# Kernel optimization log

Hardware: AMD Instinct MI355X
Metric: run time of the kernel (lower is better)

## Reference

```python
import jax, jax.numpy as jnp
import numpy as np
from jax import lax

EPS = 1e-5
DN = ('NCHW', 'OIHW', 'NCHW')


def setup_inputs() -> dict:
    key = jax.random.key(0)
    ks = jax.random.split(key, 16)
    B = 8192
    # uniform(0,1): every pixel nonzero => all voxels active => sparse conv == dense conv
    x = jax.random.uniform(ks[0], (B, 1, 28, 28), dtype=jnp.float32)

    def conv_params(kw, kb, c_in, c_out, k):
        scale = 1.0 / np.sqrt(c_in * k * k)
        w = jax.random.normal(kw, (c_out, c_in, k, k), dtype=jnp.float32) * scale
        b = jax.random.normal(kb, (c_out,), dtype=jnp.float32) * scale
        return w, b

    w0, b0 = conv_params(ks[1], ks[2], 1, 32, 3)
    w1, b1 = conv_params(ks[3], ks[4], 32, 64, 2)
    w2, b2 = conv_params(ks[5], ks[6], 64, 128, 2)
    # BatchNorm affine params (init: gamma=1, beta=0)
    g0, be0 = jnp.ones((32,), jnp.float32), jnp.zeros((32,), jnp.float32)
    g1, be1 = jnp.ones((64,), jnp.float32), jnp.zeros((64,), jnp.float32)
    g2, be2 = jnp.ones((128,), jnp.float32), jnp.zeros((128,), jnp.float32)
    w_fc = jax.random.normal(ks[7], (10, 128), dtype=jnp.float32) * (1.0 / np.sqrt(128))
    b_fc = jax.random.normal(ks[8], (10,), dtype=jnp.float32) * (1.0 / np.sqrt(128))
    return dict(x=x, w0=w0, b0=b0, g0=g0, be0=be0,
                w1=w1, b1=b1, g1=g1, be1=be1,
                w2=w2, b2=b2, g2=g2, be2=be2,
                w_fc=w_fc, b_fc=b_fc)


def _conv_bn_relu(x, w, b, g, be, stride, padding):
    # sparse conv on fully-active grid == dense conv
    y = lax.conv_general_dilated(x, w, (stride, stride), padding,
                                 dimension_numbers=DN)
    y = y + b[None, :, None, None]
    # BatchNorm1d over (N_active, C) == stats over batch+spatial (biased var)
    mean = jnp.mean(y, axis=(0, 2, 3))
    var = jnp.var(y, axis=(0, 2, 3))
    y = (y - mean[None, :, None, None]) * lax.rsqrt(var + EPS)[None, :, None, None]
    y = y * g[None, :, None, None] + be[None, :, None, None]
    return jax.nn.relu(y)


def reference(x, w0, b0, g0, be0, w1, b1, g1, be1, w2, b2, g2, be2, w_fc, b_fc):
    h = _conv_bn_relu(x, w0, b0, g0, be0, 1, 'SAME')    # (B,32,28,28)
    h = _conv_bn_relu(h, w1, b1, g1, be1, 2, 'VALID')   # (B,64,14,14)
    h = _conv_bn_relu(h, w2, b2, g2, be2, 2, 'VALID')   # (B,128,7,7)
    pooled = jnp.mean(h, axis=(2, 3))                    # AdaptiveAvgPool2d(1)+Flatten
    return pooled @ w_fc.T + b_fc                        # (B, n_classes)
```

## Files before the change

### kernel.cpp

```cpp
#include <hip/hip_runtime.h>
#include <hip/hip_bf16.h>

typedef __bf16 bf16x8 __attribute__((ext_vector_type(8)));
typedef float  f32x4  __attribute__((ext_vector_type(4)));
typedef float  f32x2  __attribute__((ext_vector_type(2)));

#define BSZ 8192

__device__ __constant__ int d_base2[9] = {0, 5, 9, 13, 16, 19, 21, 23, 24};

__global__ __launch_bounds__(256) void k_stats0(const float* __restrict__ x,
                                                float* __restrict__ part0,
                                                const float* __restrict__ w1,
                                                const float* __restrict__ w2,
                                                __bf16* __restrict__ w1b,
                                                __bf16* __restrict__ w2b) {
    __shared__ float sred[4 * 59];
    const int tid = threadIdx.x;
    {
        int t = blockIdx.x * 256 + tid;
        if (t < 8192) {
            int oc = t >> 7, k = t & 127, c = k & 31, d = k >> 5;
            w1b[t] = (__bf16)w1[oc * 128 + c * 4 + d];
        }
        if (t < 32768) {
            int oc = t >> 8, k = t & 255, c = k & 63, d = k >> 6;
            w2b[t] = (__bf16)w2[oc * 256 + c * 4 + d];
        }
    }
    const int base2[9] = {0, 5, 9, 13, 16, 19, 21, 23, 24};
    const int rsz[9]   = {5, 4, 4, 3, 3, 2, 2, 1, 1};
    f32x2 a2[25];
    float ax[9];
#pragma unroll
    for (int i = 0; i < 25; i++) a2[i] = (f32x2){0.f, 0.f};
#pragma unroll
    for (int i = 0; i < 9; i++) ax[i] = 0.f;
    const int total = BSZ * 784;
    for (int p = blockIdx.x * 256 + tid; p < total; p += gridDim.x * 256) {
        int b = p / 784, pix = p - b * 784;
        int y = pix / 28, xx = pix - y * 28;
        const float* xb = x + (long)b * 784;
        float nv[9];
#pragma unroll
        for (int dy = 0; dy < 3; dy++) {
            int yy = y + dy - 1;
#pragma unroll
            for (int dx = 0; dx < 3; dx++) {
                int x2 = xx + dx - 1;
                nv[dy * 3 + dx] = (yy >= 0 && yy < 28 && x2 >= 0 && x2 < 28) ? xb[yy * 28 + x2] : 0.f;
            }
        }
#pragma unroll
        for (int t = 0; t < 9; t++) {
            float vt = nv[t];
            ax[t] += vt;
            f32x2 vv = {vt, vt};
#pragma unroll
            for (int pp2 = 0; pp2 < 5; pp2++) {
                if (pp2 < rsz[t]) {
                    int u = t + 2 * pp2;
                    f32x2 nn = {nv[u], (u + 1 < 9) ? nv[u + 1] : 0.f};
                    a2[base2[t] + pp2] = __builtin_elementwise_fma(vv, nn, a2[base2[t] + pp2]);
                }
            }
        }
    }
    float outv[59];
#pragma unroll
    for (int i = 0; i < 50; i++) outv[i] = a2[i >> 1][i & 1];
#pragma unroll
    for (int i = 0; i < 9; i++) outv[50 + i] = ax[i];
#pragma unroll
    for (int i = 0; i < 59; i++) {
        float v = outv[i];
        v += __shfl_xor(v, 1);  v += __shfl_xor(v, 2);  v += __shfl_xor(v, 4);
        v += __shfl_xor(v, 8);  v += __shfl_xor(v, 16); v += __shfl_xor(v, 32);
        outv[i] = v;
    }
    const int l = tid & 63, w = tid >> 6;
    if (l == 0) {
#pragma unroll
        for (int i = 0; i < 59; i++) sred[w * 59 + i] = outv[i];
    }
    __syncthreads();
    if (tid < 59)
        part0[blockIdx.x * 64 + tid] = sred[tid] + sred[59 + tid] + sred[118 + tid] + sred[177 + tid];
}

__global__ void k_fin0(const float* __restrict__ part0, const float* __restrict__ w0,
                       const float* __restrict__ g0, const float* __restrict__ be0,
                       float* __restrict__ abc0) {
    __shared__ float red[4 * 59];
    int t = threadIdx.x, c = t & 63, g = t >> 6;
    if (c < 59) {
        float acc = 0.f;
        for (int i = g; i < 1024; i += 4) acc += part0[i * 64 + c];
        red[g * 59 + c] = acc;
    }
    __syncthreads();
    if (t < 59) red[t] = red[t] + red[59 + t] + red[118 + t] + red[177 + t];
    __syncthreads();
    if (t < 32) {
        const int base2[9] = {0, 5, 9, 13, 16, 19, 21, 23, 24};
        float wv[9];
#pragma unroll
        for (int tap = 0; tap < 9; tap++) wv[tap] = w0[t * 9 + tap];
        float sum = 0.f, sq = 0.f;
#pragma unroll
        for (int ta = 0; ta < 9; ta++) {
            sum = fmaf(wv[ta], red[50 + ta], sum);
#pragma unroll
            for (int u = ta; u < 9; u++) {
                float coef = (u == ta) ? 1.f : 2.f;
                float Mv = red[2 * base2[ta] + (u - ta)];
                sq = fmaf(coef * wv[ta] * wv[u], Mv, sq);
            }
        }
        float cnt = (float)BSZ * 784.f;
        float mean = sum / cnt;
        float var = sq / cnt - mean * mean;
        float A = g0[t] * rsqrtf(var + 1e-5f);
#pragma unroll
        for (int tap = 0; tap < 9; tap++)
            abc0[(t >> 3) * 72 + tap * 8 + (t & 7)] = A * wv[tap];
        abc0[288 + t] = be0[t] - mean * A;
    }
}

__global__ __launch_bounds__(256) void k_conv01(const float* __restrict__ x,
                                                const float* __restrict__ abc0,
                                                const __bf16* __restrict__ w1b,
                                                __bf16* __restrict__ h1,
                                                float* __restrict__ part1) {
    __shared__ float xs[30 * 30];
    __shared__ __attribute__((aligned(16))) __bf16 sAt[2][16 * 136];
    const int tid = threadIdx.x;
    if (tid < 116) {
        int idx;
        if (tid < 30)      idx = tid;
        else if (tid < 60) idx = 29 * 30 + (tid - 30);
        else if (tid < 88) idx = (tid - 60 + 1) * 30;
        else               idx = (tid - 88 + 1) * 30 + 29;
        xs[idx] = 0.f;
    }
    const int pgu = __builtin_amdgcn_readfirstlane(tid >> 6);
    const f32x2* wfp = (const f32x2*)(abc0 + pgu * 72);
    f32x2 wf2[36];
#pragma unroll
    for (int i = 0; i < 36; i++) wf2[i] = wfp[i];
    const f32x2* c2p = (const f32x2*)(abc0 + 288 + pgu * 8);
    f32x2 c2[4];
#pragma unroll
    for (int j = 0; j < 4; j++) c2[j] = c2p[j];

    const int pi = tid & 15, pd = (tid >> 4) & 3;
    const int w = tid >> 6, l = tid & 63, q = l >> 4, n = l & 15;
    const int oc = w * 16 + n;
    bf16x8 fbv[4];
#pragma unroll
    for (int kc = 0; kc < 4; kc++)
        fbv[kc] = *(const bf16x8*)&w1b[oc * 128 + kc * 32 + q * 8];
    const f32x2 zero2 = {0.f, 0.f};

    for (int img = 0; img < 4; img++) {
        const int b = blockIdx.x * 4 + img;
        const f32x4* xb4 = (const f32x4*)(x + (long)b * 784);
        if (tid < 196) {
            int yy = tid / 7, xx4 = (tid - yy * 7) * 4;
            f32x4 v4 = xb4[tid];
            float* dst = &xs[(yy + 1) * 30 + xx4 + 1];
            dst[0] = v4[0]; dst[1] = v4[1]; dst[2] = v4[2]; dst[3] = v4[3];
        }
        __syncthreads();
        f32x2 st_s = zero2, st_q = zero2;
        __bf16* hb = h1 + (long)b * 12544 + (q * 4) * 64 + oc;
        for (int mt = 0; mt < 13; mt++) {
            __bf16* dst = &sAt[mt & 1][pi * 136 + pd * 32 + pgu * 8];
            int m = mt * 16 + pi;
            bf16x8 pk;
            if (m < 196) {
                int my = m / 14, mx = m - my * 14;
                int y0 = my * 2 + (pd >> 1), x0 = mx * 2 + (pd & 1);
                float nv[9];
#pragma unroll
                for (int dy = 0; dy < 3; dy++)
#pragma unroll
                    for (int dx = 0; dx < 3; dx++)
                        nv[dy * 3 + dx] = xs[(y0 + dy) * 30 + x0 + dx];
                f32x2 a2[4];
#pragma unroll
                for (int j = 0; j < 4; j++) a2[j] = c2[j];
#pragma unroll
                for (int t = 0; t < 9; t++) {
                    f32x2 vv = {nv[t], nv[t]};
#pragma unroll
                    for (int j = 0; j < 4; j++)
                        a2[j] = __builtin_elementwise_fma(vv, wf2[t * 4 + j], a2[j]);
                }
#pragma unroll
                for (int j = 0; j < 4; j++) {
                    f32x2 mv = __builtin_elementwise_max(a2[j], zero2);
                    pk[2 * j]     = (__bf16)mv[0];
                    pk[2 * j + 1] = (__bf16)mv[1];
                }
            } else {
#pragma unroll
                for (int j = 0; j < 8; j++) pk[j] = (__bf16)0.0f;
            }
            *(bf16x8*)dst = pk;
            __syncthreads();
            const __bf16* sa = &sAt[mt & 1][n * 136 + q * 8];
            f32x4 acc = {0.f, 0.f, 0.f, 0.f};
#pragma unroll
            for (int kc = 0; kc < 4; kc++) {
                bf16x8 fav = *(const bf16x8*)&sa[kc * 32];
                acc = __builtin_amdgcn_mfma_f32_16x16x32_bf16(fav, fbv[kc], acc, 0, 0, 0);
            }
            bool valid = (mt < 12) | (q == 0);
            __bf16* hp = hb + mt * 16 * 64;
            float fv[4];
#pragma unroll
            for (int r = 0; r < 4; r++) {
                __bf16 hv = (__bf16)acc[r];
                if (valid) hp[r * 64] = hv;
                fv[r] = (float)hv;
            }
            f32x2 f01 = {fv[0], fv[1]}, f23 = {fv[2], fv[3]};
            st_s = st_s + f01; st_s = st_s + f23;
            st_q = __builtin_elementwise_fma(f01, f01, st_q);
            st_q = __builtin_elementwise_fma(f23, f23, st_q);
        }
        float ssum = st_s[0] + st_s[1], ssq = st_q[0] + st_q[1];
        ssum += __shfl_xor(ssum, 16); ssum += __shfl_xor(ssum, 32);
        ssq  += __shfl_xor(ssq, 16);  ssq  += __shfl_xor(ssq, 32);
        if (l < 16) {
            part1[(long)oc * BSZ + b] = ssum;
            part1[(long)(64 + oc) * BSZ + b] = ssq;
        }
    }
}

__global__ __launch_bounds__(256) void k_redfin(const float* __restrict__ part,
                                                const float* __restrict__ g,
                                                const float* __restrict__ be,
                                                float* __restrict__ abc,
                                                int C, float cnt) {
    __shared__ float s1[256], s2[256];
    const int c = blockIdx.x, tid = threadIdx.x;
    float a = 0.f, bq = 0.f;
    const float* p1 = part + (long)c * BSZ;
    const float* p2 = part + (long)(C + c) * BSZ;
    for (int i = tid; i < BSZ; i += 256) { a += p1[i]; bq += p2[i]; }
    s1[tid] = a; s2[tid] = bq;
    __syncthreads();
    for (int s = 128; s > 0; s >>= 1) {
        if (tid < s) { s1[tid] += s1[tid + s]; s2[tid] += s2[tid + s]; }
        __syncthreads();
    }
    if (tid == 0) {
        float mean = s1[0] / cnt;
        float var = s2[0] / cnt - mean * mean;
        float A = g[c] * rsqrtf(var + 1e-5f);
        abc[c] = A;
        abc[C + c] = be[c] - mean * A;
    }
}

__global__ __launch_bounds__(256) void k_conv2s(__bf16* __restrict__ h1,
                                                const __bf16* __restrict__ w2b,
                                                const float* __restrict__ abc1,
                                                float* __restrict__ part2) {
    __shared__ __attribute__((aligned(16))) __bf16 sAt[2][16 * 264];
    __shared__ __attribute__((aligned(16))) __bf16 zt[2][16 * 136];
    __shared__ float sbn1[128];
    const int tid = threadIdx.x;
    if (tid < 128) sbn1[tid] = abc1[tid];
    const int w = tid >> 6, l = tid & 63, q = l >> 4, n = l & 15;
    bf16x8 fbv[2][8];
#pragma unroll
    for (int ntl = 0; ntl < 2; ntl++) {
        int oc = (2 * w + ntl) * 16 + n;
#pragma unroll
        for (int kc = 0; kc < 8; kc++)
            fbv[ntl][kc] = *(const bf16x8*)&w2b[oc * 256 + kc * 32 + q * 8];
    }
    __syncthreads();
    const int cpb = (tid & 7) * 8;
    f32x2 A1p[4], C1p[4];
#pragma unroll
    for (int p = 0; p < 4; p++) {
        A1p[p] = (f32x2){sbn1[cpb + 2 * p], sbn1[cpb + 2 * p + 1]};
        C1p[p] = (f32x2){sbn1[64 + cpb + 2 * p], sbn1[64 + cpb + 2 * p + 1]};
    }
    const f32x2 zero2 = {0.f, 0.f};
    const int srow = tid >> 4, so = (tid & 15) * 8;

    for (int img = 0; img < 4; img++) {
        const int b = blockIdx.x * 4 + img;
        __bf16* src = h1 + (long)b * 12544;
        f32x2 st_s[2] = {zero2, zero2}, st_q[2] = {zero2, zero2};
        for (int mt = 0; mt < 4; mt++) {
            if (mt >= 2) {
                int m = (mt - 2) * 16 + srow;
                if (m < 49) {
                    bf16x8 zv = *(const bf16x8*)&zt[mt & 1][srow * 136 + so];
                    *(bf16x8*)&src[m * 128 + so] = zv;
                }
            }
#pragma unroll
            for (int it = 0; it < 2; it++) {
                int idx = it * 256 + tid;
                int rl = idx >> 5, o = (idx & 31) * 8;
                int r = mt * 16 + rl;
                bf16x8 wv;
                if (r < 49) {
                    int d = o >> 6;
                    int c = o & 63;
                    int py = r / 7, px = r - py * 7;
                    int msrc = (2 * py + (d >> 1)) * 14 + 2 * px + (d & 1);
                    bf16x8 v = *(const bf16x8*)&src[msrc * 64 + c];
#pragma unroll
                    for (int p = 0; p < 4; p++) {
                        f32x2 vf = {(float)v[2 * p], (float)v[2 * p + 1]};
                        f32x2 rr = __builtin_elementwise_fma(vf, A1p[p], C1p[p]);
                        rr = __builtin_elementwise_max(rr, zero2);
                        wv[2 * p]     = (__bf16)rr[0];
                        wv[2 * p + 1] = (__bf16)rr[1];
                    }
                } else {
#pragma unroll
                    for (int j = 0; j < 8; j++) wv[j] = (__bf16)0.0f;
                }
                *(bf16x8*)&sAt[mt & 1][rl * 264 + o] = wv;
            }
            __syncthreads();
            bf16x8 fav[8];
#pragma unroll
            for (int kc = 0; kc < 8; kc++)
                fav[kc] = *(const bf16x8*)&sAt[mt & 1][n * 264 + kc * 32 + q * 8];
#pragma unroll
            for (int ntl = 0; ntl < 2; ntl++) {
                f32x4 acc = {0.f, 0.f, 0.f, 0.f};
#pragma unroll
                for (int kc = 0; kc < 8; kc++)
                    acc = __builtin_amdgcn_mfma_f32_16x16x32_bf16(fav[kc], fbv[ntl][kc], acc, 0, 0, 0);
                float fv[4];
#pragma unroll
                for (int rr = 0; rr < 4; rr++) {
                    __bf16 hv = (__bf16)acc[rr];
                    zt[mt & 1][(q * 4 + rr) * 136 + (2 * w + ntl) * 16 + n] = hv;
                    fv[rr] = (float)hv;
                }
                f32x2 f01 = {fv[0], fv[1]}, f23 = {fv[2], fv[3]};
                st_s[ntl] = st_s[ntl] + f01; st_s[ntl] = st_s[ntl] + f23;
                st_q[ntl] = __builtin_elementwise_fma(f01, f01, st_q[ntl]);
                st_q[ntl] = __builtin_elementwise_fma(f23, f23, st_q[ntl]);
            }
        }
        __syncthreads();
        {
            int m2 = 32 + srow;
            if (m2 < 49) {
                bf16x8 zv = *(const bf16x8*)&zt[0][srow * 136 + so];
                *(bf16x8*)&src[m2 * 128 + so] = zv;
            }
            int m3 = 48 + srow;
            if (m3 < 49) {
                bf16x8 zv = *(const bf16x8*)&zt[1][srow * 136 + so];
                *(bf16x8*)&src[m3 * 128 + so] = zv;
            }
        }
#pragma unroll
        for (int ntl = 0; ntl < 2; ntl++) {
            float ssum = st_s[ntl][0] + st_s[ntl][1];
            float ssq  = st_q[ntl][0] + st_q[ntl][1];
            ssum += __shfl_xor(ssum, 16); ssum += __shfl_xor(ssum, 32);
            ssq  += __shfl_xor(ssq, 16);  ssq  += __shfl_xor(ssq, 32);
            if (l < 16) {
                int oc = (2 * w + ntl) * 16 + l;
                part2[(long)oc * BSZ + b] = ssum;
                part2[(long)(128 + oc) * BSZ + b] = ssq;
            }
        }
    }
}

__global__ __launch_bounds__(256) void k_final(const __bf16* __restrict__ z2,
                                               const float* __restrict__ abc2,
                                               const float* __restrict__ wfc,
                                               const float* __restrict__ bfc,
                                               float* __restrict__ out) {
    __shared__ float sbn2[256];
    __shared__ float pp[16 * 128];
    __shared__ float pooled[128];
    __shared__ float fcred[80];
    const int tid = threadIdx.x;
    sbn2[tid] = abc2[tid];
    __syncthreads();
    const int g = tid & 15, c0 = g * 8, rg = tid >> 4;
    f32x2 A2p[4], C2p[4];
#pragma unroll
    for (int p = 0; p < 4; p++) {
        A2p[p] = (f32x2){sbn2[c0 + 2 * p], sbn2[c0 + 2 * p + 1]};
        C2p[p] = (f32x2){sbn2[128 + c0 + 2 * p], sbn2[128 + c0 + 2 * p + 1]};
    }
    const f32x2 zero2 = {0.f, 0.f};
    for (int img = 0; img < 4; img++) {
        const int b = blockIdx.x * 4 + img;
        const __bf16* src = z2 + (long)b * 12544;
        f32x2 acc2[4];
#pragma unroll
        for (int p = 0; p < 4; p++) acc2[p] = zero2;
        for (int rr = rg; rr < 49; rr += 16) {
            bf16x8 v = *(const bf16x8*)&src[rr * 128 + c0];
#pragma unroll
            for (int p = 0; p < 4; p++) {
                f32x2 vf = {(float)v[2 * p], (float)v[2 * p + 1]};
                f32x2 t0 = __builtin_elementwise_fma(vf, A2p[p], C2p[p]);
                t0 = __builtin_elementwise_max(t0, zero2);
                acc2[p] = acc2[p] + t0;
            }
        }
        f32x4 lo = {acc2[0][0], acc2[0][1], acc2[1][0], acc2[1][1]};
        f32x4 hi = {acc2[2][0], acc2[2][1], acc2[3][0], acc2[3][1]};
        *(f32x4*)&pp[rg * 128 + c0]     = lo;
        *(f32x4*)&pp[rg * 128 + c0 + 4] = hi;
        __syncthreads();
        if (tid < 128) {
            float s = 0.f;
#pragma unroll
            for (int r = 0; r < 16; r++) s += pp[r * 128 + tid];
            pooled[tid] = s * (1.f / 49.f);
        }
        __syncthreads();
        if (tid < 80) {
            int o = tid >> 3, s = tid & 7;
            float a = 0.f;
#pragma unroll
            for (int j = 0; j < 16; j++) a = fmaf(pooled[s * 16 + j], wfc[o * 128 + s * 16 + j], a);
            fcred[tid] = a;
        }
        __syncthreads();
        if (tid < 10) {
            float a = bfc[tid];
#pragma unroll
            for (int s = 0; s < 8; s++) a += fcred[tid * 8 + s];
            out[(long)b * 10 + tid] = a;
        }
    }
}

extern "C" void kernel_launch(void* const* d_in, const int* in_sizes, int n_in,
                              void* d_out, int out_size, void* d_ws, size_t ws_size,
                              hipStream_t stream) {
    const float* x   = (const float*)d_in[0];
    const float* w0  = (const float*)d_in[1];
    const float* g0  = (const float*)d_in[3];
    const float* be0 = (const float*)d_in[4];
    const float* w1  = (const float*)d_in[5];
    const float* g1  = (const float*)d_in[7];
    const float* be1 = (const float*)d_in[8];
    const float* w2  = (const float*)d_in[9];
    const float* g2  = (const float*)d_in[11];
    const float* be2 = (const float*)d_in[12];
    const float* wfc = (const float*)d_in[13];
    const float* bfc = (const float*)d_in[14];
    float* out = (float*)d_out;

    float* ws    = (float*)d_ws;
    float* part0 = ws;
    float* abc0  = part0 + 1024 * 64;
    float* part1 = abc0 + 320;
    float* abc1  = part1 + 128 * BSZ;
    float* part2 = abc1 + 128;
    float* abc2  = part2 + 256 * BSZ;
    __bf16* w1b  = (__bf16*)(abc2 + 256);
    __bf16* w2b  = w1b + 8192;
    __bf16* h1   = w2b + 32768;

    k_stats0<<<dim3(1024), dim3(256), 0, stream>>>(x, part0, w1, w2, w1b, w2b);
    k_fin0<<<dim3(1), dim3(256), 0, stream>>>(part0, w0, g0, be0, abc0);
    k_conv01<<<dim3(BSZ / 4), dim3(256), 0, stream>>>(x, abc0, w1b, h1, part1);
    k_redfin<<<dim3(64), dim3(256), 0, stream>>>(part1, g1, be1, abc1, 64, (float)(BSZ * 196));
    k_conv2s<<<dim3(BSZ / 4), dim3(256), 0, stream>>>(h1, w2b, abc1, part2);
    k_redfin<<<dim3(128), dim3(256), 0, stream>>>(part2, g2, be2, abc2, 128, (float)(BSZ * 49));
    k_final<<<dim3(BSZ / 4), dim3(256), 0, stream>>>(h1, abc2, wfc, bfc, out);
}
```

Baseline: 410.3 us.

## Fuse all stages into one cooperative persistent kernel with grid syncs

Replaces the seven separate kernel launches with a single cooperative kernel of 512 persistent blocks. Each block handles 16 images, and stages are separated by grid.sync. Per-image partial statistics are now accumulated per block, which shrinks the partial buffers and the final reductions. This removes launch gaps and per-launch overhead. In exchange, grid-wide barriers are added and occupancy is capped by the 4-blocks-per-CU launch bound, which may reduce latency hiding during the heavy conv stages.

```diff
diff --git a/kernel.cpp b/kernel.cpp
--- a/kernel.cpp
+++ b/kernel.cpp
@@ -1,374 +1,390 @@
 #include <hip/hip_runtime.h>
 #include <hip/hip_bf16.h>
+#include <hip/hip_cooperative_groups.h>
+
+namespace cg = cooperative_groups;
 
 typedef __bf16 bf16x8 __attribute__((ext_vector_type(8)));
 typedef float  f32x4  __attribute__((ext_vector_type(4)));
 typedef float  f32x2  __attribute__((ext_vector_type(2)));
 
 #define BSZ 8192
-
-__device__ __constant__ int d_base2[9] = {0, 5, 9, 13, 16, 19, 21, 23, 24};
-
-__global__ __launch_bounds__(256) void k_stats0(const float* __restrict__ x,
-                                                float* __restrict__ part0,
-                                                const float* __restrict__ w1,
-                                                const float* __restrict__ w2,
-                                                __bf16* __restrict__ w1b,
-                                                __bf16* __restrict__ w2b) {
-    __shared__ float sred[4 * 59];
-    const int tid = threadIdx.x;
+#define NBLK 512
+#define IPB  16
+
+__global__ __launch_bounds__(256, 4) void k_mega(const float* __restrict__ x,
+                                                 const float* __restrict__ w0,
+                                                 const float* __restrict__ g0,
+                                                 const float* __restrict__ be0,
+                                                 const float* __restrict__ w1,
+                                                 const float* __restrict__ g1,
+                                                 const float* __restrict__ be1,
+                                                 const float* __restrict__ w2,
+                                                 const float* __restrict__ g2,
+                                                 const float* __restrict__ be2,
+                                                 const float* __restrict__ wfc,
+                                                 const float* __restrict__ bfc,
+                                                 float* __restrict__ out,
+                                                 float* __restrict__ wsf) {
+    __shared__ __attribute__((aligned(16))) unsigned char smem[26112];
+    cg::grid_group grid = cg::this_grid();
+    const int tid = threadIdx.x, blk = blockIdx.x;
+
+    float* part0 = wsf;
+    float* abc0  = part0 + NBLK * 64;
+    float* part1 = abc0 + 320;
+    float* abc1  = part1 + 128 * NBLK;
+    float* part2 = abc1 + 128;
+    float* abc2  = part2 + 256 * NBLK;
+    __bf16* w1b  = (__bf16*)(abc2 + 256);
+    __bf16* w2b  = w1b + 8192;
+    __bf16* h1   = w2b + 32768;
+
     {
-        int t = blockIdx.x * 256 + tid;
-        if (t < 8192) {
-            int oc = t >> 7, k = t & 127, c = k & 31, d = k >> 5;
-            w1b[t] = (__bf16)w1[oc * 128 + c * 4 + d];
-        }
-        if (t < 32768) {
-            int oc = t >> 8, k = t & 255, c = k & 63, d = k >> 6;
-            w2b[t] = (__bf16)w2[oc * 256 + c * 4 + d];
-        }
-    }
-    const int base2[9] = {0, 5, 9, 13, 16, 19, 21, 23, 24};
-    const int rsz[9]   = {5, 4, 4, 3, 3, 2, 2, 1, 1};
-    f32x2 a2[25];
-    float ax[9];
-#pragma unroll
-    for (int i = 0; i < 25; i++) a2[i] = (f32x2){0.f, 0.f};
-#pragma unroll
-    for (int i = 0; i < 9; i++) ax[i] = 0.f;
-    const int total = BSZ * 784;
-    for (int p = blockIdx.x * 256 + tid; p < total; p += gridDim.x * 256) {
-        int b = p / 784, pix = p - b * 784;
-        int y = pix / 28, xx = pix - y * 28;
-        const float* xb = x + (long)b * 784;
-        float nv[9];
-#pragma unroll
-        for (int dy = 0; dy < 3; dy++) {
-            int yy = y + dy - 1;
-#pragma unroll
-            for (int dx = 0; dx < 3; dx++) {
-                int x2 = xx + dx - 1;
-                nv[dy * 3 + dx] = (yy >= 0 && yy < 28 && x2 >= 0 && x2 < 28) ? xb[yy * 28 + x2] : 0.f;
-            }
-        }
-#pragma unroll
-        for (int t = 0; t < 9; t++) {
-            float vt = nv[t];
-            ax[t] += vt;
-            f32x2 vv = {vt, vt};
-#pragma unroll
-            for (int pp2 = 0; pp2 < 5; pp2++) {
-                if (pp2 < rsz[t]) {
-                    int u = t + 2 * pp2;
-                    f32x2 nn = {nv[u], (u + 1 < 9) ? nv[u + 1] : 0.f};
-                    a2[base2[t] + pp2] = __builtin_elementwise_fma(vv, nn, a2[base2[t] + pp2]);
-                }
-            }
-        }
-    }
-    float outv[59];
-#pragma unroll
-    for (int i = 0; i < 50; i++) outv[i] = a2[i >> 1][i & 1];
-#pragma unroll
-    for (int i = 0; i < 9; i++) outv[50 + i] = ax[i];
-#pragma unroll
-    for (int i = 0; i < 59; i++) {
-        float v = outv[i];
-        v += __shfl_xor(v, 1);  v += __shfl_xor(v, 2);  v += __shfl_xor(v, 4);
-        v += __shfl_xor(v, 8);  v += __shfl_xor(v, 16); v += __shfl_xor(v, 32);
-        outv[i] = v;
-    }
-    const int l = tid & 63, w = tid >> 6;
-    if (l == 0) {
-#pragma unroll
-        for (int i = 0; i < 59; i++) sred[w * 59 + i] = outv[i];
-    }
-    __syncthreads();
-    if (tid < 59)
-        part0[blockIdx.x * 64 + tid] = sred[tid] + sred[59 + tid] + sred[118 + tid] + sred[177 + tid];
-}
-
-__global__ void k_fin0(const float* __restrict__ part0, const float* __restrict__ w0,
-                       const float* __restrict__ g0, const float* __restrict__ be0,
-                       float* __restrict__ abc0) {
-    __shared__ float red[4 * 59];
-    int t = threadIdx.x, c = t & 63, g = t >> 6;
-    if (c < 59) {
-        float acc = 0.f;
-        for (int i = g; i < 1024; i += 4) acc += part0[i * 64 + c];
-        red[g * 59 + c] = acc;
-    }
-    __syncthreads();
-    if (t < 59) red[t] = red[t] + red[59 + t] + red[118 + t] + red[177 + t];
-    __syncthreads();
-    if (t < 32) {
+        float* sred = (float*)smem;
+        for (int t = blk * 256 + tid; t < 32768; t += NBLK * 256) {
+            if (t < 8192) {
+                int oc = t >> 7, k = t & 127, c = k & 31, d = k >> 5;
+                w1b[t] = (__bf16)w1[oc * 128 + c * 4 + d];
+            }
+            {
+                int oc = t >> 8, k = t & 255, c = k & 63, d = k >> 6;
+                w2b[t] = (__bf16)w2[oc * 256 + c * 4 + d];
+            }
+        }
         const int base2[9] = {0, 5, 9, 13, 16, 19, 21, 23, 24};
-        float wv[9];
-#pragma unroll
-        for (int tap = 0; tap < 9; tap++) wv[tap] = w0[t * 9 + tap];
-        float sum = 0.f, sq = 0.f;
-#pragma unroll
-        for (int ta = 0; ta < 9; ta++) {
-            sum = fmaf(wv[ta], red[50 + ta], sum);
-#pragma unroll
-            for (int u = ta; u < 9; u++) {
-                float coef = (u == ta) ? 1.f : 2.f;
-                float Mv = red[2 * base2[ta] + (u - ta)];
-                sq = fmaf(coef * wv[ta] * wv[u], Mv, sq);
-            }
-        }
-        float cnt = (float)BSZ * 784.f;
-        float mean = sum / cnt;
-        float var = sq / cnt - mean * mean;
-        float A = g0[t] * rsqrtf(var + 1e-5f);
-#pragma unroll
-        for (int tap = 0; tap < 9; tap++)
-            abc0[(t >> 3) * 72 + tap * 8 + (t & 7)] = A * wv[tap];
-        abc0[288 + t] = be0[t] - mean * A;
-    }
-}
-
-__global__ __launch_bounds__(256) void k_conv01(const float* __restrict__ x,
-                                                const float* __restrict__ abc0,
-                                                const __bf16* __restrict__ w1b,
-                                                __bf16* __restrict__ h1,
-                                                float* __restrict__ part1) {
-    __shared__ float xs[30 * 30];
-    __shared__ __attribute__((aligned(16))) __bf16 sAt[2][16 * 136];
-    const int tid = threadIdx.x;
-    if (tid < 116) {
-        int idx;
-        if (tid < 30)      idx = tid;
-        else if (tid < 60) idx = 29 * 30 + (tid - 30);
-        else if (tid < 88) idx = (tid - 60 + 1) * 30;
-        else               idx = (tid - 88 + 1) * 30 + 29;
-        xs[idx] = 0.f;
-    }
-    const int pgu = __builtin_amdgcn_readfirstlane(tid >> 6);
-    const f32x2* wfp = (const f32x2*)(abc0 + pgu * 72);
-    f32x2 wf2[36];
-#pragma unroll
-    for (int i = 0; i < 36; i++) wf2[i] = wfp[i];
-    const f32x2* c2p = (const f32x2*)(abc0 + 288 + pgu * 8);
-    f32x2 c2[4];
-#pragma unroll
-    for (int j = 0; j < 4; j++) c2[j] = c2p[j];
-
-    const int pi = tid & 15, pd = (tid >> 4) & 3;
-    const int w = tid >> 6, l = tid & 63, q = l >> 4, n = l & 15;
-    const int oc = w * 16 + n;
-    bf16x8 fbv[4];
-#pragma unroll
-    for (int kc = 0; kc < 4; kc++)
-        fbv[kc] = *(const bf16x8*)&w1b[oc * 128 + kc * 32 + q * 8];
-    const f32x2 zero2 = {0.f, 0.f};
-
-    for (int img = 0; img < 4; img++) {
-        const int b = blockIdx.x * 4 + img;
-        const f32x4* xb4 = (const f32x4*)(x + (long)b * 784);
-        if (tid < 196) {
-            int yy = tid / 7, xx4 = (tid - yy * 7) * 4;
-            f32x4 v4 = xb4[tid];
-            float* dst = &xs[(yy + 1) * 30 + xx4 + 1];
-            dst[0] = v4[0]; dst[1] = v4[1]; dst[2] = v4[2]; dst[3] = v4[3];
-        }
-        __syncthreads();
+        const int rsz[9]   = {5, 4, 4, 3, 3, 2, 2, 1, 1};
+        f32x2 a2[25];
+        float ax[9];
+#pragma unroll
+        for (int i = 0; i < 25; i++) a2[i] = (f32x2){0.f, 0.f};
+#pragma unroll
+        for (int i = 0; i < 9; i++) ax[i] = 0.f;
+        const int total = BSZ * 784;
+        for (int p = blk * 256 + tid; p < total; p += NBLK * 256) {
+            int b = p / 784, pix = p - b * 784;
+            int y = pix / 28, xx = pix - y * 28;
+            const float* xb = x + (long)b * 784;
+            float nv[9];
+#pragma unroll
+            for (int dy = 0; dy < 3; dy++) {
+                int yy = y + dy - 1;
+#pragma unroll
+                for (int dx = 0; dx < 3; dx++) {
+                    int x2 = xx + dx - 1;
+                    nv[dy * 3 + dx] = (yy >= 0 && yy < 28 && x2 >= 0 && x2 < 28) ? xb[yy * 28 + x2] : 0.f;
+                }
+            }
+#pragma unroll
+            for (int t2 = 0; t2 < 9; t2++) {
+                float vt = nv[t2];
+                ax[t2] += vt;
+                f32x2 vv = {vt, vt};
+#pragma unroll
+                for (int pp2 = 0; pp2 < 5; pp2++) {
+                    if (pp2 < rsz[t2]) {
+                        int u = t2 + 2 * pp2;
+                        f32x2 nn = {nv[u], (u + 1 < 9) ? nv[u + 1] : 0.f};
+                        a2[base2[t2] + pp2] = __builtin_elementwise_fma(vv, nn, a2[base2[t2] + pp2]);
+                    }
+                }
+            }
+        }
+        float outv[59];
+#pragma unroll
+        for (int i = 0; i < 50; i++) outv[i] = a2[i >> 1][i & 1];
+#pragma unroll
+        for (int i = 0; i < 9; i++) outv[50 + i] = ax[i];
+#pragma unroll
+        for (int i = 0; i < 59; i++) {
+            float v = outv[i];
+            v += __shfl_xor(v, 1);  v += __shfl_xor(v, 2);  v += __shfl_xor(v, 4);
+            v += __shfl_xor(v, 8);  v += __shfl_xor(v, 16); v += __shfl_xor(v, 32);
+            outv[i] = v;
+        }
+        const int l = tid & 63, w = tid >> 6;
+        if (l == 0) {
+#pragma unroll
+            for (int i = 0; i < 59; i++) sred[w * 59 + i] = outv[i];
+        }
+        __syncthreads();
+        if (tid < 59)
+            part0[blk * 64 + tid] = sred[tid] + sred[59 + tid] + sred[118 + tid] + sred[177 + tid];
+    }
+    grid.sync();
+
+    if (blk == 0) {
+        float* red = (float*)smem;
+        int t = tid, c = t & 63, g = t >> 6;
+        if (c < 59) {
+            float acc = 0.f;
+            for (int i = g; i < NBLK; i += 4) acc += part0[i * 64 + c];
+            red[g * 59 + c] = acc;
+        }
+        __syncthreads();
+        if (t < 59) red[t] = red[t] + red[59 + t] + red[118 + t] + red[177 + t];
+        __syncthreads();
+        if (t < 32) {
+            const int base2[9] = {0, 5, 9, 13, 16, 19, 21, 23, 24};
+            float wv[9];
+#pragma unroll
+            for (int tap = 0; tap < 9; tap++) wv[tap] = w0[t * 9 + tap];
+            float sum = 0.f, sq = 0.f;
+#pragma unroll
+            for (int ta = 0; ta < 9; ta++) {
+                sum = fmaf(wv[ta], red[50 + ta], sum);
+#pragma unroll
+                for (int u = ta; u < 9; u++) {
+                    float coef = (u == ta) ? 1.f : 2.f;
+                    float Mv = red[2 * base2[ta] + (u - ta)];
+                    sq = fmaf(coef * wv[ta] * wv[u], Mv, sq);
+                }
+            }
+            float cnt = (float)BSZ * 784.f;
+            float mean = sum / cnt;
+            float var = sq / cnt - mean * mean;
+            float A = g0[t] * rsqrtf(var + 1e-5f);
+#pragma unroll
+            for (int tap = 0; tap < 9; tap++)
+                abc0[(t >> 3) * 72 + tap * 8 + (t & 7)] = A * wv[tap];
+            abc0[288 + t] = be0[t] - mean * A;
+        }
+    }
+    grid.sync();
+
+    {
+        float* xs = (float*)smem;
+        __bf16* sAt = (__bf16*)(smem + 3600);
+        if (tid < 116) {
+            int idx;
+            if (tid < 30)      idx = tid;
+            else if (tid < 60) idx = 29 * 30 + (tid - 30);
+            else if (tid < 88) idx = (tid - 60 + 1) * 30;
+            else               idx = (tid - 88 + 1) * 30 + 29;
+            xs[idx] = 0.f;
+        }
+        const int pgu = __builtin_amdgcn_readfirstlane(tid >> 6);
+        const f32x2* wfp = (const f32x2*)(abc0 + pgu * 72);
+        f32x2 wf2[36];
+#pragma unroll
+        for (int i = 0; i < 36; i++) wf2[i] = wfp[i];
+        const f32x2* c2p = (const f32x2*)(abc0 + 288 + pgu * 8);
+        f32x2 c2[4];
+#pragma unroll
+        for (int j = 0; j < 4; j++) c2[j] = c2p[j];
+        const int pi = tid & 15, pd = (tid >> 4) & 3;
+        const int w = tid >> 6, l = tid & 63, q = l >> 4, n = l & 15;
+        const int oc = w * 16 + n;
+        bf16x8 fbv[4];
+#pragma unroll
+        for (int kc = 0; kc < 4; kc++)
+            fbv[kc] = *(const bf16x8*)&w1b[oc * 128 + kc * 32 + q * 8];
+        const f32x2 zero2 = {0.f, 0.f};
         f32x2 st_s = zero2, st_q = zero2;
-        __bf16* hb = h1 + (long)b * 12544 + (q * 4) * 64 + oc;
-        for (int mt = 0; mt < 13; mt++) {
-            __bf16* dst = &sAt[mt & 1][pi * 136 + pd * 32 + pgu * 8];
-            int m = mt * 16 + pi;
-            bf16x8 pk;
-            if (m < 196) {
-                int my = m / 14, mx = m - my * 14;
-                int y0 = my * 2 + (pd >> 1), x0 = mx * 2 + (pd & 1);
-                float nv[9];
-#pragma unroll
-                for (int dy = 0; dy < 3; dy++)
-#pragma unroll
-                    for (int dx = 0; dx < 3; dx++)
-                        nv[dy * 3 + dx] = xs[(y0 + dy) * 30 + x0 + dx];
-                f32x2 a2[4];
-#pragma unroll
-                for (int j = 0; j < 4; j++) a2[j] = c2[j];
-#pragma unroll
-                for (int t = 0; t < 9; t++) {
-                    f32x2 vv = {nv[t], nv[t]};
-#pragma unroll
-                    for (int j = 0; j < 4; j++)
-                        a2[j] = __builtin_elementwise_fma(vv, wf2[t * 4 + j], a2[j]);
-                }
-#pragma unroll
-                for (int j = 0; j < 4; j++) {
-                    f32x2 mv = __builtin_elementwise_max(a2[j], zero2);
-                    pk[2 * j]     = (__bf16)mv[0];
-                    pk[2 * j + 1] = (__bf16)mv[1];
-                }
-            } else {
-#pragma unroll
-                for (int j = 0; j < 8; j++) pk[j] = (__bf16)0.0f;
-            }
-            *(bf16x8*)dst = pk;
-            __syncthreads();
-            const __bf16* sa = &sAt[mt & 1][n * 136 + q * 8];
-            f32x4 acc = {0.f, 0.f, 0.f, 0.f};
-#pragma unroll
-            for (int kc = 0; kc < 4; kc++) {
-                bf16x8 fav = *(const bf16x8*)&sa[kc * 32];
-                acc = __builtin_amdgcn_mfma_f32_16x16x32_bf16(fav, fbv[kc], acc, 0, 0, 0);
-            }
-            bool valid = (mt < 12) | (q == 0);
-            __bf16* hp = hb + mt * 16 * 64;
-            float fv[4];
-#pragma unroll
-            for (int r = 0; r < 4; r++) {
-                __bf16 hv = (__bf16)acc[r];
-                if (valid) hp[r * 64] = hv;
-                fv[r] = (float)hv;
-            }
-            f32x2 f01 = {fv[0], fv[1]}, f23 = {fv[2], fv[3]};
-            st_s = st_s + f01; st_s = st_s + f23;
-            st_q = __builtin_elementwise_fma(f01, f01, st_q);
-            st_q = __builtin_elementwise_fma(f23, f23, st_q);
+
+        for (int img = 0; img < IPB; img++) {
+            const int b = blk * IPB + img;
+            const f32x4* xb4 = (const f32x4*)(x + (long)b * 784);
+            if (tid < 196) {
+                int yy = tid / 7, xx4 = (tid - yy * 7) * 4;
+                f32x4 v4 = xb4[tid];
+                float* dst = &xs[(yy + 1) * 30 + xx4 + 1];
+                dst[0] = v4[0]; dst[1] = v4[1]; dst[2] = v4[2]; dst[3] = v4[3];
+            }
+            __syncthreads();
+            __bf16* hb = h1 + (long)b * 12544 + (q * 4) * 64 + oc;
+            for (int mt = 0; mt < 13; mt++) {
+                __bf16* dst = &sAt[(mt & 1) * 2176 + pi * 136 + pd * 32 + pgu * 8];
+                int m = mt * 16 + pi;
+                bf16x8 pk;
+                if (m < 196) {
+                    int my = m / 14, mx = m - my * 14;
+                    int y0 = my * 2 + (pd >> 1), x0 = mx * 2 + (pd & 1);
+                    float nv[9];
+#pragma unroll
+                    for (int dy = 0; dy < 3; dy++)
+#pragma unroll
+                        for (int dx = 0; dx < 3; dx++)
+                            nv[dy * 3 + dx] = xs[(y0 + dy) * 30 + x0 + dx];
+                    f32x2 a2[4];
+#pragma unroll
+                    for (int j = 0; j < 4; j++) a2[j] = c2[j];
+#pragma unroll
+                    for (int t = 0; t < 9; t++) {
+                        f32x2 vv = {nv[t], nv[t]};
+#pragma unroll
+                        for (int j = 0; j < 4; j++)
+                            a2[j] = __builtin_elementwise_fma(vv, wf2[t * 4 + j], a2[j]);
+                    }
+#pragma unroll
+                    for (int j = 0; j < 4; j++) {
+                        f32x2 mv = __builtin_elementwise_max(a2[j], zero2);
+                        pk[2 * j]     = (__bf16)mv[0];
+                        pk[2 * j + 1] = (__bf16)mv[1];
+                    }
+                } else {
+#pragma unroll
+                    for (int j = 0; j < 8; j++) pk[j] = (__bf16)0.0f;
+                }
+                *(bf16x8*)dst = pk;
+                __syncthreads();
+                const __bf16* sa = &sAt[(mt & 1) * 2176 + n * 136 + q * 8];
+                f32x4 acc = {0.f, 0.f, 0.f, 0.f};
+#pragma unroll
+                for (int kc = 0; kc < 4; kc++) {
+                    bf16x8 fav = *(const bf16x8*)&sa[kc * 32];
+                    acc = __builtin_amdgcn_mfma_f32_16x16x32_bf16(fav, fbv[kc], acc, 0, 0, 0);
+                }
+                bool valid = (mt < 12) | (q == 0);
+                __bf16* hp = hb + mt * 16 * 64;
+                float fv[4];
+#pragma unroll
+                for (int r = 0; r < 4; r++) {
+                    __bf16 hv = (__bf16)acc[r];
+                    if (valid) hp[r * 64] = hv;
+                    fv[r] = (float)hv;
+                }
+                f32x2 f01 = {fv[0], fv[1]}, f23 = {fv[2], fv[3]};
+                st_s = st_s + f01; st_s = st_s + f23;
+                st_q = __builtin_elementwise_fma(f01, f01, st_q);
+                st_q = __builtin_elementwise_fma(f23, f23, st_q);
+            }
+            __syncthreads();
         }
         float ssum = st_s[0] + st_s[1], ssq = st_q[0] + st_q[1];
         ssum += __shfl_xor(ssum, 16); ssum += __shfl_xor(ssum, 32);
         ssq  += __shfl_xor(ssq, 16);  ssq  += __shfl_xor(ssq, 32);
         if (l < 16) {
-            part1[(long)oc * BSZ + b] = ssum;
-            part1[(long)(64 + oc) * BSZ + b] = ssq;
-        }
-    }
-}
-
-__global__ __launch_bounds__(256) void k_redfin(const float* __restrict__ part,
-                                                const float* __restrict__ g,
-                                                const float* __restrict__ be,
-                                                float* __restrict__ abc,
-                                                int C, float cnt) {
-    __shared__ float s1[256], s2[256];
-    const int c = blockIdx.x, tid = threadIdx.x;
-    float a = 0.f, bq = 0.f;
-    const float* p1 = part + (long)c * BSZ;
-    const float* p2 = part + (long)(C + c) * BSZ;
-    for (int i = tid; i < BSZ; i += 256) { a += p1[i]; bq += p2[i]; }
-    s1[tid] = a; s2[tid] = bq;
-    __syncthreads();
-    for (int s = 128; s > 0; s >>= 1) {
-        if (tid < s) { s1[tid] += s1[tid + s]; s2[tid] += s2[tid + s]; }
-        __syncthreads();
-    }
-    if (tid == 0) {
-        float mean = s1[0] / cnt;
-        float var = s2[0] / cnt - mean * mean;
-        float A = g[c] * rsqrtf(var + 1e-5f);
-        abc[c] = A;
-        abc[C + c] = be[c] - mean * A;
-    }
-}
-
-__global__ __launch_bounds__(256) void k_conv2s(__bf16* __restrict__ h1,
-                                                const __bf16* __restrict__ w2b,
-                                                const float* __restrict__ abc1,
-                                                float* __restrict__ part2) {
-    __shared__ __attribute__((aligned(16))) __bf16 sAt[2][16 * 264];
-    __shared__ __attribute__((aligned(16))) __bf16 zt[2][16 * 136];
-    __shared__ float sbn1[128];
-    const int tid = threadIdx.x;
-    if (tid < 128) sbn1[tid] = abc1[tid];
-    const int w = tid >> 6, l = tid & 63, q = l >> 4, n = l & 15;
-    bf16x8 fbv[2][8];
-#pragma unroll
-    for (int ntl = 0; ntl < 2; ntl++) {
-        int oc = (2 * w + ntl) * 16 + n;
-#pragma unroll
-        for (int kc = 0; kc < 8; kc++)
-            fbv[ntl][kc] = *(const bf16x8*)&w2b[oc * 256 + kc * 32 + q * 8];
-    }
-    __syncthreads();
-    const int cpb = (tid & 7) * 8;
-    f32x2 A1p[4], C1p[4];
-#pragma unroll
-    for (int p = 0; p < 4; p++) {
-        A1p[p] = (f32x2){sbn1[cpb + 2 * p], sbn1[cpb + 2 * p + 1]};
-        C1p[p] = (f32x2){sbn1[64 + cpb + 2 * p], sbn1[64 + cpb + 2 * p + 1]};
-    }
-    const f32x2 zero2 = {0.f, 0.f};
-    const int srow = tid >> 4, so = (tid & 15) * 8;
-
-    for (int img = 0; img < 4; img++) {
-        const int b = blockIdx.x * 4 + img;
-        __bf16* src = h1 + (long)b * 12544;
+            part1[(long)oc * NBLK + blk] = ssum;
+            part1[(long)(64 + oc) * NBLK + blk] = ssq;
+        }
+    }
+    grid.sync();
+
+    if (blk < 64) {
+        float* s1 = (float*)smem;
+        float* s2 = (float*)(smem + 1024);
+        const int c = blk;
+        float a = 0.f, bq = 0.f;
+        const float* p1 = part1 + (long)c * NBLK;
+        const float* p2 = part1 + (long)(64 + c) * NBLK;
+        for (int i = tid; i < NBLK; i += 256) { a += p1[i]; bq += p2[i]; }
+        s1[tid] = a; s2[tid] = bq;
+        __syncthreads();
+        for (int s = 128; s > 0; s >>= 1) {
+            if (tid < s) { s1[tid] += s1[tid + s]; s2[tid] += s2[tid + s]; }
+            __syncthreads();
+        }
+        if (tid == 0) {
+            float cnt = (float)(BSZ * 196);
+            float mean = s1[0] / cnt;
+            float var = s2[0] / cnt - mean * mean;
+            float A = g1[c] * rsqrtf(var + 1e-5f);
+            abc1[c] = A;
+            abc1[64 + c] = be1[c] - mean * A;
+        }
+    }
+    grid.sync();
+
+    {
+        __bf16* sAt = (__bf16*)smem;
+        __bf16* zt  = (__bf16*)(smem + 16896);
+        float* sbn1 = (float*)(smem + 25600);
+        if (tid < 128) sbn1[tid] = abc1[tid];
+        const int w = tid >> 6, l = tid & 63, q = l >> 4, n = l & 15;
+        bf16x8 fbv[2][8];
+#pragma unroll
+        for (int ntl = 0; ntl < 2; ntl++) {
+            int oc = (2 * w + ntl) * 16 + n;
+#pragma unroll
+            for (int kc = 0; kc < 8; kc++)
+                fbv[ntl][kc] = *(const bf16x8*)&w2b[oc * 256 + kc * 32 + q * 8];
+        }
+        __syncthreads();
+        const int cpb = (tid & 7) * 8;
+        f32x2 A1p[4], C1p[4];
+#pragma unroll
+        for (int p = 0; p < 4; p++) {
+            A1p[p] = (f32x2){sbn1[cpb + 2 * p], sbn1[cpb + 2 * p + 1]};
+            C1p[p] = (f32x2){sbn1[64 + cpb + 2 * p], sbn1[64 + cpb + 2 * p + 1]};
+        }
+        const f32x2 zero2 = {0.f, 0.f};
+        const int srow = tid >> 4, so = (tid & 15) * 8;
         f32x2 st_s[2] = {zero2, zero2}, st_q[2] = {zero2, zero2};
-        for (int mt = 0; mt < 4; mt++) {
-            if (mt >= 2) {
-                int m = (mt - 2) * 16 + srow;
-                if (m < 49) {
-                    bf16x8 zv = *(const bf16x8*)&zt[mt & 1][srow * 136 + so];
-                    *(bf16x8*)&src[m * 128 + so] = zv;
-                }
-            }
-#pragma unroll
-            for (int it = 0; it < 2; it++) {
-                int idx = it * 256 + tid;
-                int rl = idx >> 5, o = (idx & 31) * 8;
-                int r = mt * 16 + rl;
-                bf16x8 wv;
-                if (r < 49) {
-                    int d = o >> 6;
-                    int c = o & 63;
-                    int py = r / 7, px = r - py * 7;
-                    int msrc = (2 * py + (d >> 1)) * 14 + 2 * px + (d & 1);
-                    bf16x8 v = *(const bf16x8*)&src[msrc * 64 + c];
-#pragma unroll
-                    for (int p = 0; p < 4; p++) {
-                        f32x2 vf = {(float)v[2 * p], (float)v[2 * p + 1]};
-                        f32x2 rr = __builtin_elementwise_fma(vf, A1p[p], C1p[p]);
-                        rr = __builtin_elementwise_max(rr, zero2);
-                        wv[2 * p]     = (__bf16)rr[0];
-                        wv[2 * p + 1] = (__bf16)rr[1];
+
+        for (int img = 0; img < IPB; img++) {
+            const int b = blk * IPB + img;
+            __bf16* src = h1 + (long)b * 12544;
+            for (int mt = 0; mt < 4; mt++) {
+                if (mt >= 2) {
+                    int m = (mt - 2) * 16 + srow;
+                    if (m < 49) {
+                        bf16x8 zv = *(const bf16x8*)&zt[(mt & 1) * 2176 + srow * 136 + so];
+                        *(bf16x8*)&src[m * 128 + so] = zv;
                     }
-                } else {
-#pragma unroll
-                    for (int j = 0; j < 8; j++) wv[j] = (__bf16)0.0f;
-                }
-                *(bf16x8*)&sAt[mt & 1][rl * 264 + o] = wv;
-            }
-            __syncthreads();
-            bf16x8 fav[8];
-#pragma unroll
-            for (int kc = 0; kc < 8; kc++)
-                fav[kc] = *(const bf16x8*)&sAt[mt & 1][n * 264 + kc * 32 + q * 8];
-#pragma unroll
-            for (int ntl = 0; ntl < 2; ntl++) {
-                f32x4 acc = {0.f, 0.f, 0.f, 0.f};
+                }
+#pragma unroll
+                for (int it = 0; it < 2; it++) {
+                    int idx = it * 256 + tid;
+                    int rl = idx >> 5, o = (idx & 31) * 8;
+                    int r = mt * 16 + rl;
+                    bf16x8 wv;
+                    if (r < 49) {
+                        int d = o >> 6;
+                        int c = o & 63;
+                        int py = r / 7, px = r - py * 7;
+                        int msrc = (2 * py + (d >> 1)) * 14 + 2 * px + (d & 1);
+                        bf16x8 v = *(const bf16x8*)&src[msrc * 64 + c];
+#pragma unroll
+                        for (int p = 0; p < 4; p++) {
+                            f32x2 vf = {(float)v[2 * p], (float)v[2 * p + 1]};
+                            f32x2 rr = __builtin_elementwise_fma(vf, A1p[p], C1p[p]);
+                            rr = __builtin_elementwise_max(rr, zero2);
+                            wv[2 * p]     = (__bf16)rr[0];
+                            wv[2 * p + 1] = (__bf16)rr[1];
+                        }
+                    } else {
+#pragma unroll
+                        for (int j = 0; j < 8; j++) wv[j] = (__bf16)0.0f;
+                    }
+                    *(bf16x8*)&sAt[(mt & 1) * 4224 + rl * 264 + o] = wv;
+                }
+                __syncthreads();
+                bf16x8 fav[8];
 #pragma unroll
                 for (int kc = 0; kc < 8; kc++)
-                    acc = __builtin_amdgcn_mfma_f32_16x16x32_bf16(fav[kc], fbv[ntl][kc], acc, 0, 0, 0);
-                float fv[4];
-#pragma unroll
-                for (int rr = 0; rr < 4; rr++) {
-                    __bf16 hv = (__bf16)acc[rr];
-                    zt[mt & 1][(q * 4 + rr) * 136 + (2 * w + ntl) * 16 + n] = hv;
-                    fv[rr] = (float)hv;
-                }
-                f32x2 f01 = {fv[0], fv[1]}, f23 = {fv[2], fv[3]};
-                st_s[ntl] = st_s[ntl] + f01; st_s[ntl] = st_s[ntl] + f23;
-                st_q[ntl] = __builtin_elementwise_fma(f01, f01, st_q[ntl]);
-                st_q[ntl] = __builtin_elementwise_fma(f23, f23, st_q[ntl]);
-            }
-        }
-        __syncthreads();
-        {
-            int m2 = 32 + srow;
-            if (m2 < 49) {
-                bf16x8 zv = *(const bf16x8*)&zt[0][srow * 136 + so];
-                *(bf16x8*)&src[m2 * 128 + so] = zv;
-            }
-            int m3 = 48 + srow;
-            if (m3 < 49) {
-                bf16x8 zv = *(const bf16x8*)&zt[1][srow * 136 + so];
-                *(bf16x8*)&src[m3 * 128 + so] = zv;
+                    fav[kc] = *(const bf16x8*)&sAt[(mt & 1) * 4224 + n * 264 + kc * 32 + q * 8];
+#pragma unroll
+                for (int ntl = 0; ntl < 2; ntl++) {
+                    f32x4 acc = {0.f, 0.f, 0.f, 0.f};
+#pragma unroll
+                    for (int kc = 0; kc < 8; kc++)
+                        acc = __builtin_amdgcn_mfma_f32_16x16x32_bf16(fav[kc], fbv[ntl][kc], acc, 0, 0, 0);
+                    float fv[4];
+#pragma unroll
+                    for (int rr = 0; rr < 4; rr++) {
+                        __bf16 hv = (__bf16)acc[rr];
+                        zt[(mt & 1) * 2176 + (q * 4 + rr) * 136 + (2 * w + ntl) * 16 + n] = hv;
+                        fv[rr] = (float)hv;
+                    }
+                    f32x2 f01 = {fv[0], fv[1]}, f23 = {fv[2], fv[3]};
+                    st_s[ntl] = st_s[ntl] + f01; st_s[ntl] = st_s[ntl] + f23;
+                    st_q[ntl] = __builtin_elementwise_fma(f01, f01, st_q[ntl]);
+                    st_q[ntl] = __builtin_elementwise_fma(f23, f23, st_q[ntl]);
+                }
+            }
+            __syncthreads();
+            {
+                int m2 = 32 + srow;
+                if (m2 < 49) {
+                    bf16x8 zv = *(const bf16x8*)&zt[srow * 136 + so];
+                    *(bf16x8*)&src[m2 * 128 + so] = zv;
+                }
+                int m3 = 48 + srow;
+                if (m3 < 49) {
+                    bf16x8 zv = *(const bf16x8*)&zt[2176 + srow * 136 + so];
+                    *(bf16x8*)&src[m3 * 128 + so] = zv;
+                }
             }
         }
 #pragma unroll
@@ -379,74 +395,96 @@
             ssq  += __shfl_xor(ssq, 16);  ssq  += __shfl_xor(ssq, 32);
             if (l < 16) {
                 int oc = (2 * w + ntl) * 16 + l;
-                part2[(long)oc * BSZ + b] = ssum;
-                part2[(long)(128 + oc) * BSZ + b] = ssq;
-            }
-        }
-    }
-}
-
-__global__ __launch_bounds__(256) void k_final(const __bf16* __restrict__ z2,
-                                               const float* __restrict__ abc2,
-                                               const float* __restrict__ wfc,
-                                               const float* __restrict__ bfc,
-                                               float* __restrict__ out) {
-    __shared__ float sbn2[256];
-    __shared__ float pp[16 * 128];
-    __shared__ float pooled[128];
-    __shared__ float fcred[80];
-    const int tid = threadIdx.x;
-    sbn2[tid] = abc2[tid];
-    __syncthreads();
-    const int g = tid & 15, c0 = g * 8, rg = tid >> 4;
-    f32x2 A2p[4], C2p[4];
-#pragma unroll
-    for (int p = 0; p < 4; p++) {
-        A2p[p] = (f32x2){sbn2[c0 + 2 * p], sbn2[c0 + 2 * p + 1]};
-        C2p[p] = (f32x2){sbn2[128 + c0 + 2 * p], sbn2[128 + c0 + 2 * p + 1]};
-    }
-    const f32x2 zero2 = {0.f, 0.f};
-    for (int img = 0; img < 4; img++) {
-        const int b = blockIdx.x * 4 + img;
-        const __bf16* src = z2 + (long)b * 12544;
-        f32x2 acc2[4];
-#pragma unroll
-        for (int p = 0; p < 4; p++) acc2[p] = zero2;
-        for (int rr = rg; rr < 49; rr += 16) {
-            bf16x8 v = *(const bf16x8*)&src[rr * 128 + c0];
-#pragma unroll
-            for (int p = 0; p < 4; p++) {
-                f32x2 vf = {(float)v[2 * p], (float)v[2 * p + 1]};
-                f32x2 t0 = __builtin_elementwise_fma(vf, A2p[p], C2p[p]);
-                t0 = __builtin_elementwise_max(t0, zero2);
-                acc2[p] = acc2[p] + t0;
-            }
-        }
-        f32x4 lo = {acc2[0][0], acc2[0][1], acc2[1][0], acc2[1][1]};
-        f32x4 hi = {acc2[2][0], acc2[2][1], acc2[3][0], acc2[3][1]};
-        *(f32x4*)&pp[rg * 128 + c0]     = lo;
-        *(f32x4*)&pp[rg * 128 + c0 + 4] = hi;
-        __syncthreads();
-        if (tid < 128) {
-            float s = 0.f;
-#pragma unroll
-            for (int r = 0; r < 16; r++) s += pp[r * 128 + tid];
-            pooled[tid] = s * (1.f / 49.f);
-        }
-        __syncthreads();
-        if (tid < 80) {
-            int o = tid >> 3, s = tid & 7;
-            float a = 0.f;
-#pragma unroll
-            for (int j = 0; j < 16; j++) a = fmaf(pooled[s * 16 + j], wfc[o * 128 + s * 16 + j], a);
-            fcred[tid] = a;
-        }
-        __syncthreads();
-        if (tid < 10) {
-            float a = bfc[tid];
-#pragma unroll
-            for (int s = 0; s < 8; s++) a += fcred[tid * 8 + s];
-            out[(long)b * 10 + tid] = a;
+                part2[(long)oc * NBLK + blk] = ssum;
+                part2[(long)(128 + oc) * NBLK + blk] = ssq;
+            }
+        }
+    }
+    grid.sync();
+
+    if (blk < 128) {
+        float* s1 = (float*)smem;
+        float* s2 = (float*)(smem + 1024);
+        const int c = blk;
+        float a = 0.f, bq = 0.f;
+        const float* p1 = part2 + (long)c * NBLK;
+        const float* p2 = part2 + (long)(128 + c) * NBLK;
+        for (int i = tid; i < NBLK; i += 256) { a += p1[i]; bq += p2[i]; }
+        s1[tid] = a; s2[tid] = bq;
+        __syncthreads();
+        for (int s = 128; s > 0; s >>= 1) {
+            if (tid < s) { s1[tid] += s1[tid + s]; s2[tid] += s2[tid + s]; }
+            __syncthreads();
+        }
+        if (tid == 0) {
+            float cnt = (float)(BSZ * 49);
+            float mean = s1[0] / cnt;
+            float var = s2[0] / cnt - mean * mean;
+            float A = g2[c] * rsqrtf(var + 1e-5f);
+            abc2[c] = A;
+            abc2[128 + c] = be2[c] - mean * A;
+        }
+    }
+    grid.sync();
+
+    {
+        float* sbn2 = (float*)smem;
+        float* pp   = (float*)(smem + 1024);
+        float* pooled = (float*)(smem + 9216);
+        float* fcred  = (float*)(smem + 9728);
+        sbn2[tid] = abc2[tid];
+        __syncthreads();
+        const int g = tid & 15, c0 = g * 8, rg = tid >> 4;
+        f32x2 A2p[4], C2p[4];
+#pragma unroll
+        for (int p = 0; p < 4; p++) {
+            A2p[p] = (f32x2){sbn2[c0 + 2 * p], sbn2[c0 + 2 * p + 1]};
+            C2p[p] = (f32x2){sbn2[128 + c0 + 2 * p], sbn2[128 + c0 + 2 * p + 1]};
+        }
+        const f32x2 zero2 = {0.f, 0.f};
+        for (int img = 0; img < IPB; img++) {
+            const int b = blk * IPB + img;
+            const __bf16* src = h1 + (long)b * 12544;
+            f32x2 acc2[4];
+#pragma unroll
+            for (int p = 0; p < 4; p++) acc2[p] = zero2;
+            for (int rr = rg; rr < 49; rr += 16) {
+                bf16x8 v = *(const bf16x8*)&src[rr * 128 + c0];
+#pragma unroll
+                for (int p = 0; p < 4; p++) {
+                    f32x2 vf = {(float)v[2 * p], (float)v[2 * p + 1]};
+                    f32x2 t0 = __builtin_elementwise_fma(vf, A2p[p], C2p[p]);
+                    t0 = __builtin_elementwise_max(t0, zero2);
+                    acc2[p] = acc2[p] + t0;
+                }
+            }
+            f32x4 lo = {acc2[0][0], acc2[0][1], acc2[1][0], acc2[1][1]};
+            f32x4 hi = {acc2[2][0], acc2[2][1], acc2[3][0], acc2[3][1]};
+            *(f32x4*)&pp[rg * 128 + c0]     = lo;
+            *(f32x4*)&pp[rg * 128 + c0 + 4] = hi;
+            __syncthreads();
+            if (tid < 128) {
+                float s = 0.f;
+#pragma unroll
+                for (int r = 0; r < 16; r++) s += pp[r * 128 + tid];
+                pooled[tid] = s * (1.f / 49.f);
+            }
+            __syncthreads();
+            if (tid < 80) {
+                int o = tid >> 3, s = tid & 7;
+                float a = 0.f;
+#pragma unroll
+                for (int j = 0; j < 16; j++) a = fmaf(pooled[s * 16 + j], wfc[o * 128 + s * 16 + j], a);
+                fcred[tid] = a;
+            }
+            __syncthreads();
+            if (tid < 10) {
+                float a = bfc[tid];
+#pragma unroll
+                for (int s = 0; s < 8; s++) a += fcred[tid * 8 + s];
+                out[(long)b * 10 + tid] = a;
+            }
+            __syncthreads();
         }
     }
 }
@@ -467,23 +505,11 @@
     const float* wfc = (const float*)d_in[13];
     const float* bfc = (const float*)d_in[14];
     float* out = (float*)d_out;
-
-    float* ws    = (float*)d_ws;
-    float* part0 = ws;
-    float* abc0  = part0 + 1024 * 64;
-    float* part1 = abc0 + 320;
-    float* abc1  = part1 + 128 * BSZ;
-    float* part2 = abc1 + 128;
-    float* abc2  = part2 + 256 * BSZ;
-    __bf16* w1b  = (__bf16*)(abc2 + 256);
-    __bf16* w2b  = w1b + 8192;
-    __bf16* h1   = w2b + 32768;
-
-    k_stats0<<<dim3(1024), dim3(256), 0, stream>>>(x, part0, w1, w2, w1b, w2b);
-    k_fin0<<<dim3(1), dim3(256), 0, stream>>>(part0, w0, g0, be0, abc0);
-    k_conv01<<<dim3(BSZ / 4), dim3(256), 0, stream>>>(x, abc0, w1b, h1, part1);
-    k_redfin<<<dim3(64), dim3(256), 0, stream>>>(part1, g1, be1, abc1, 64, (float)(BSZ * 196));
-    k_conv2s<<<dim3(BSZ / 4), dim3(256), 0, stream>>>(h1, w2b, abc1, part2);
-    k_redfin<<<dim3(128), dim3(256), 0, stream>>>(part2, g2, be2, abc2, 128, (float)(BSZ * 49));
-    k_final<<<dim3(BSZ / 4), dim3(256), 0, stream>>>(h1, abc2, wfc, bfc, out);
+    float* wsf = (float*)d_ws;
+
+    void* args[] = {(void*)&x, (void*)&w0, (void*)&g0, (void*)&be0,
+                    (void*)&w1, (void*)&g1, (void*)&be1,
+                    (void*)&w2, (void*)&g2, (void*)&be2,
+                    (void*)&wfc, (void*)&bfc, (void*)&out, (void*)&wsf};
+    hipLaunchCooperativeKernel((void*)k_mega, dim3(NBLK), dim3(256), args, 0, stream);
 }
```

Result: slower. 1.442 ms (+251.4%).
